# Kernel optimization log

Measured on AMD Instinct MI355X. Metric: run time of the kernel, lower is better.

The kernel has to match this reference:

```python
import jax, jax.numpy as jnp
import numpy as np

THRESH = 0.33
EPS = 1e-10


def _ternarize(x, max_val):
    # x / (max(|x|)+eps) thresholded to {-1, 0, +1}
    n = x / (max_val + EPS)
    return jnp.where(n > THRESH, 1, jnp.where(n < -THRESH, -1, 0)).astype(jnp.int32)


def setup_inputs() -> dict:
    key = jax.random.key(0)
    k1, k2 = jax.random.split(key)
    V, D = 131072, 1024
    qs = jax.random.normal(k1, (D,), dtype=jnp.float32)
    # embedding init: xavier-ish normal + small noise, then row-normalized (as in _initialize_embeddings)
    W = jax.random.normal(k2, (V, D), dtype=jnp.float32)
    W = W / jnp.linalg.norm(W, axis=1, keepdims=True)
    return {"quantum_state": qs, "embedding_weight": W, "top_k": 16}


def reference(quantum_state, embedding_weight, top_k):
    V, D = embedding_weight.shape
    # --- coarse pass: ternary quantization of query and full table ---
    t_state = _ternarize(quantum_state, jnp.max(jnp.abs(quantum_state)))          # [D]
    t_emb = _ternarize(embedding_weight,
                       jnp.max(jnp.abs(embedding_weight), axis=1, keepdims=True))  # [V,D]
    eq = (t_state[None, :] == t_emb)                                               # [V,D]
    # matches contribute +1, mismatches -0.5 (matches.sum - 0.5*mismatches.sum)
    ternary_sim = jnp.sum(jnp.where(eq, 1.0, -0.5), axis=1)                        # [V]
    k3 = min(top_k * 3, V)
    _, top_ternary_idx = jax.lax.top_k(ternary_sim, k3)                            # [k3]
    # --- refine pass: cosine similarity on candidates ---
    cand = embedding_weight[top_ternary_idx]                                       # [k3,D]
    q_n = quantum_state / (jnp.linalg.norm(quantum_state) + 1e-12)
    c_n = cand / (jnp.linalg.norm(cand, axis=1, keepdims=True) + 1e-12)
    refined = c_n @ q_n                                                            # [k3]
    top_scores, top_local = jax.lax.top_k(refined, top_k)                          # [top_k]
    top_global = top_ternary_idx[top_local]
    return top_scores, top_global
```

## Files before the change

### kernel.cpp

```cpp
#include <hip/hip_runtime.h>
#include <stdint.h>

#define VROWS 131072
#define DIM   1024
#define TTHRESH 0.33f
#define TEPS    1e-10f
#define KB_BLOCKS 2048
#define REG_BLOCKS 832
#define NHB   32
#define CAP   16384
#define CAPL  4096

#define MBOUND ((double)TTHRESH + 0x1p-26)

#define GCOUNT_OFF 1024
#define TVAL_OFF  1028
#define MATCH_OFF 4096
#define PART_OFF  (MATCH_OFF + 4 * VROWS)
#define KEYS_OFF  ((PART_OFF + 4 * NHB * 1025 + 7) & ~7)

typedef float f32x4 __attribute__((ext_vector_type(4)));

__device__ __forceinline__ float max4abs(f32x4 a) {
    return fmaxf(fmaxf(fabsf(a.x), fabsf(a.y)), fmaxf(fabsf(a.z), fabsf(a.w)));
}

__device__ __forceinline__ float boundary(float d) {
    double md = MBOUND * (double)d;
    float r = (float)md;
    if (!((double)r >= md)) r = __int_as_float(__float_as_int(r) + 1);
    return r;
}

#define SLOT(x, j) { \
    unsigned long long bp = __ballot((x) >= r); \
    unsigned long long bn = __ballot((x) <= nr); \
    unsigned long long b0 = ~(bp | bn); \
    cnt += (int)__popcll((bp & MP[j]) | (bn & MN[j]) | (b0 & ~(MP[j] | MN[j]))); }

template <bool NT>
__device__ __forceinline__ f32x4 ldW(const f32x4* p) {
    if (NT) return __builtin_nontemporal_load(p);
    return *p;
}

template <bool NT>
__device__ __forceinline__ void rows16(const float* __restrict__ W, int row0, int lane,
                                       const unsigned long long* MP, const unsigned long long* MN,
                                       int* __restrict__ matches) {
    const f32x4* p = (const f32x4*)(W + (size_t)row0 * DIM) + lane;
    f32x4 c0 = ldW<NT>(p), c1 = ldW<NT>(p + 64), c2 = ldW<NT>(p + 128), c3 = ldW<NT>(p + 192);
    f32x4 n0 = c0, n1 = c1, n2 = c2, n3 = c3;
#pragma unroll 1
    for (int i = 0; i < 16; ++i) {
        if (i < 15) {
            const f32x4* pn = (const f32x4*)(W + (size_t)(row0 + i + 1) * DIM) + lane;
            n0 = ldW<NT>(pn); n1 = ldW<NT>(pn + 64); n2 = ldW<NT>(pn + 128); n3 = ldW<NT>(pn + 192);
        }
        float m = fmaxf(fmaxf(max4abs(c0), max4abs(c1)), fmaxf(max4abs(c2), max4abs(c3)));
        for (int s = 1; s < 64; s <<= 1) m = fmaxf(m, __shfl_xor(m, s));
        float r = boundary(m + TEPS), nr = -r;
        int cnt = 0;
        SLOT(c0.x, 0)  SLOT(c0.y, 1)  SLOT(c0.z, 2)  SLOT(c0.w, 3)
        SLOT(c1.x, 4)  SLOT(c1.y, 5)  SLOT(c1.z, 6)  SLOT(c1.w, 7)
        SLOT(c2.x, 8)  SLOT(c2.y, 9)  SLOT(c2.z, 10) SLOT(c2.w, 11)
        SLOT(c3.x, 12) SLOT(c3.y, 13) SLOT(c3.z, 14) SLOT(c3.w, 15)
        if (lane == 0) matches[row0 + i] = cnt;
        c0 = n0; c1 = n1; c2 = n2; c3 = n3;
    }
}

__global__ __launch_bounds__(256, 8) void kB_coarse(const float* __restrict__ W,
                                                    const float* __restrict__ q,
                                                    int* __restrict__ matches) {
    int t = threadIdx.x;
    int wave = t >> 6, lane = t & 63;

    const f32x4* q4 = (const f32x4*)q;
    f32x4 qv0 = q4[lane], qv1 = q4[64 + lane], qv2 = q4[128 + lane], qv3 = q4[192 + lane];
    float mq = fmaxf(fmaxf(max4abs(qv0), max4abs(qv1)), fmaxf(max4abs(qv2), max4abs(qv3)));
    for (int s = 1; s < 64; s <<= 1) mq = fmaxf(mq, __shfl_xor(mq, s));
    float rq = boundary(mq + TEPS), nrq = -rq;
    unsigned long long MP[16], MN[16];
#pragma unroll
    for (int j = 0; j < 4; ++j) {
        f32x4 v = (j == 0) ? qv0 : (j == 1) ? qv1 : (j == 2) ? qv2 : qv3;
        MP[j * 4 + 0] = __ballot(v.x >= rq);  MN[j * 4 + 0] = __ballot(v.x <= nrq);
        MP[j * 4 + 1] = __ballot(v.y >= rq);  MN[j * 4 + 1] = __ballot(v.y <= nrq);
        MP[j * 4 + 2] = __ballot(v.z >= rq);  MN[j * 4 + 2] = __ballot(v.z <= nrq);
        MP[j * 4 + 3] = __ballot(v.w >= rq);  MN[j * 4 + 3] = __ballot(v.w <= nrq);
    }

    int bb = (blockIdx.x * 997) & (KB_BLOCKS - 1);
    int row0 = bb * 64 + wave * 16;
    if (bb < REG_BLOCKS) {
        rows16<false>(W, row0, lane, MP, MN, matches);
    } else {
        rows16<true>(W, row0, lane, MP, MN, matches);
    }
}

__global__ __launch_bounds__(1024) void kHist(const int* __restrict__ matches,
                                              int* __restrict__ partials,
                                              int* __restrict__ gcount) {
    __shared__ int h[1025];
    int t = threadIdx.x;
    if (t == 0) h[1024] = 0;
    if (blockIdx.x == 0 && t == 0) *gcount = 0;
    h[t] = 0;
    __syncthreads();
    int gid = blockIdx.x * 1024 + t;
    int4 m4 = ((const int4*)matches)[gid];
    atomicAdd(&h[m4.x], 1);
    atomicAdd(&h[m4.y], 1);
    atomicAdd(&h[m4.z], 1);
    atomicAdd(&h[m4.w], 1);
    __syncthreads();
    int* dst = partials + blockIdx.x * 1025;
    dst[t] = h[t];
    if (t == 0) dst[1024] = h[1024];
}

__global__ __launch_bounds__(1024) void kGather(const int* __restrict__ matches,
                                                const int* __restrict__ partials,
                                                const int* __restrict__ topk,
                                                unsigned long long* __restrict__ keys,
                                                int* __restrict__ gcount,
                                                int* __restrict__ tval) {
    __shared__ int S[2048];
    __shared__ int sT;
    int t = threadIdx.x;

    int K = *topk;
    if (K < 1) K = 1;
    if (K > 64) K = 64;
    int k3 = 3 * K;
    if (k3 > VROWS) k3 = VROWS;

    int hb = 0, hb1 = 0;
    for (int k = 0; k < NHB; ++k) {
        hb += partials[k * 1025 + t];
        if (t == 0) hb1 += partials[k * 1025 + 1024];
    }
    S[t] = hb;
    S[1024 + t] = (t == 0) ? hb1 : 0;
    __syncthreads();

    for (int s = 1; s < 2048; s <<= 1) {
        int a = S[t] + ((t + s < 2048) ? S[t + s] : 0);
        int b = S[1024 + t] + ((1024 + t + s < 2048) ? S[1024 + t + s] : 0);
        __syncthreads();
        S[t] = a;
        S[1024 + t] = b;
        __syncthreads();
    }
    if (S[t] >= k3 && S[t + 1] < k3) sT = t;
    if (t == 0 && S[1024] >= k3) sT = 1024;
    __syncthreads();
    int T = sT;
    if (t == 0) *tval = T;

    int j = blockIdx.x * 1024 + t;
    int4 m4 = ((const int4*)matches)[j];
    int rbase = j * 4;
    if (m4.x >= T) { int p = atomicAdd(gcount, 1); if (p < CAP) keys[p] = ((unsigned long long)m4.x << 32) | (unsigned int)(~(rbase)); }
    if (m4.y >= T) { int p = atomicAdd(gcount, 1); if (p < CAP) keys[p] = ((unsigned long long)m4.y << 32) | (unsigned int)(~(rbase + 1)); }
    if (m4.z >= T) { int p = atomicAdd(gcount, 1); if (p < CAP) keys[p] = ((unsigned long long)m4.z << 32) | (unsigned int)(~(rbase + 2)); }
    if (m4.w >= T) { int p = atomicAdd(gcount, 1); if (p < CAP) keys[p] = ((unsigned long long)m4.w << 32) | (unsigned int)(~(rbase + 3)); }
}

__global__ __launch_bounds__(1024) void kF_final(const float* __restrict__ W,
                                                 const float* __restrict__ q,
                                                 const int* __restrict__ topk,
                                                 const int* __restrict__ matches,
                                                 const unsigned long long* __restrict__ keys,
                                                 const int* __restrict__ gcount,
                                                 const int* __restrict__ tval,
                                                 float* __restrict__ out) {
    __shared__ __align__(16) float qs[DIM];
    __shared__ float redf[1024];
    __shared__ unsigned long long kl[CAPL];
    __shared__ int sel[192];
    __shared__ float refined[192];
    __shared__ float sQn;
    __shared__ int sG;
    int t = threadIdx.x;

    if (t < 256) ((float4*)qs)[t] = ((const float4*)q)[t];
    __syncthreads();

    float qv = qs[t];
    redf[t] = qv * qv;
    __syncthreads();
    for (int s = 512; s > 0; s >>= 1) {
        if (t < s) redf[t] += redf[t + s];
        __syncthreads();
    }
    if (t == 0) sQn = sqrtf(redf[0]) + 1e-12f;

    int K = *topk;
    if (K < 1) K = 1;
    if (K > 64) K = 64;
    int k3 = 3 * K;
    if (k3 > VROWS) k3 = VROWS;

    int G = *gcount;
    if (G <= CAPL) {
        if (t < G) kl[t] = keys[t];
        if (t == 0) sG = G;
    } else {
        if (t == 0) {
            int T = *tval;
            int n = 0;
            for (int v = 0; v < VROWS && n < k3; ++v)
                if (matches[v] > T) kl[n++] = ((unsigned long long)matches[v] << 32) | (unsigned int)(~v);
            for (int v = 0; v < VROWS && n < k3; ++v)
                if (matches[v] == T) kl[n++] = ((unsigned long long)matches[v] << 32) | (unsigned int)(~v);
            sG = n;
        }
    }
    __syncthreads();
    G = sG;

    for (int i = t; i < G; i += 1024) {
        unsigned long long ki = kl[i];
        int rank = 0;
        for (int j = 0; j < G; ++j) rank += (kl[j] > ki) ? 1 : 0;
        if (rank < k3) sel[rank] = (int)(~(unsigned int)ki);
    }
    __syncthreads();

    int wave = t >> 6, lane = t & 63;
    float qn = sQn;
    for (int i = wave; i < k3; i += 16) {
        int row = sel[i];
        const float4* Wr = (const float4*)(W + (size_t)row * DIM);
        float dot = 0.f, ss = 0.f;
        for (int j2 = 0; j2 < 4; ++j2) {
            float4 a = Wr[j2 * 64 + lane];
            float4 b = ((const float4*)qs)[j2 * 64 + lane];
            dot += a.x * b.x + a.y * b.y + a.z * b.z + a.w * b.w;
            ss  += a.x * a.x + a.y * a.y + a.z * a.z + a.w * a.w;
        }
        for (int s = 1; s < 64; s <<= 1) {
            dot += __shfl_xor(dot, s);
            ss  += __shfl_xor(ss, s);
        }
        if (lane == 0) refined[i] = dot / ((sqrtf(ss) + 1e-12f) * qn);
    }
    __syncthreads();

    if (t < k3) {
        float rv = refined[t];
        int rank = 0;
        for (int j = 0; j < k3; ++j)
            rank += ((refined[j] > rv) || (refined[j] == rv && j < t)) ? 1 : 0;
        if (rank < K) {
            out[rank] = rv;
            out[K + rank] = (float)sel[t];
        }
    }
}

extern "C" void kernel_launch(void* const* d_in, const int* in_sizes, int n_in,
                              void* d_out, int out_size, void* d_ws, size_t ws_size,
                              hipStream_t stream) {
    const float* q = (const float*)d_in[0];
    const float* W = (const float*)d_in[1];
    const int* topk = (const int*)d_in[2];
    float* out = (float*)d_out;
    char* ws = (char*)d_ws;

    int* gcount = (int*)(ws + GCOUNT_OFF);
    int* tval = (int*)(ws + TVAL_OFF);
    int* matches = (int*)(ws + MATCH_OFF);
    int* partials = (int*)(ws + PART_OFF);
    unsigned long long* keys = (unsigned long long*)(ws + KEYS_OFF);

    kB_coarse<<<KB_BLOCKS, 256, 0, stream>>>(W, q, matches);
    kHist<<<NHB, 1024, 0, stream>>>(matches, partials, gcount);
    kGather<<<NHB, 1024, 0, stream>>>(matches, partials, topk, keys, gcount, tval);
    kF_final<<<1, 1024, 0, stream>>>(W, q, topk, matches, keys, gcount, tval, out);
}
```

Before: 108.3 us.

## Fuse histogram, gather and final selection into one cooperative kernel

Merges the three post-coarse kernels (histogram, threshold gather, final refine/top-k) into a single cooperative launch with grid-wide syncs, removing two kernel launch boundaries. The matches vector is loaded once and reused across the hist and gather phases. It also raises the split point between register-path and the other rows16 variant in the coarse kernel. Cooperative launch adds grid.sync overhead, and the large shared-memory footprint per block (now combining all three kernels' buffers) may limit co-residency.

Result: slower. 134.9 us (+24.5%).

```diff
diff --git a/kernel.cpp b/kernel.cpp
--- a/kernel.cpp
+++ b/kernel.cpp
@@ -1,12 +1,15 @@
 #include <hip/hip_runtime.h>
+#include <hip/hip_cooperative_groups.h>
 #include <stdint.h>
+
+namespace cg = cooperative_groups;
 
 #define VROWS 131072
 #define DIM   1024
 #define TTHRESH 0.33f
 #define TEPS    1e-10f
 #define KB_BLOCKS 2048
-#define REG_BLOCKS 832
+#define REG_BLOCKS 960
 #define NHB   32
 #define CAP   16384
 #define CAPL  4096
@@ -100,42 +103,52 @@
     }
 }
 
-__global__ __launch_bounds__(1024) void kHist(const int* __restrict__ matches,
-                                              int* __restrict__ partials,
-                                              int* __restrict__ gcount) {
+__global__ __launch_bounds__(1024) void kS_select(const float* __restrict__ W,
+                                                  const float* __restrict__ q,
+                                                  const int* __restrict__ topk,
+                                                  const int* __restrict__ matches,
+                                                  int* __restrict__ partials,
+                                                  unsigned long long* __restrict__ keys,
+                                                  int* __restrict__ gcount,
+                                                  int* __restrict__ tval,
+                                                  float* __restrict__ out) {
+    cg::grid_group grid = cg::this_grid();
     __shared__ int h[1025];
+    __shared__ int S[2048];
+    __shared__ __align__(16) float qs[DIM];
+    __shared__ float redf[1024];
+    __shared__ unsigned long long kl[CAPL];
+    __shared__ int sel[192];
+    __shared__ float refined[192];
+    __shared__ int sT;
+    __shared__ float sQn;
+    __shared__ int sG;
     int t = threadIdx.x;
+    int b = blockIdx.x;
+
+    int K = *topk;
+    if (K < 1) K = 1;
+    if (K > 64) K = 64;
+    int k3 = 3 * K;
+    if (k3 > VROWS) k3 = VROWS;
+
     if (t == 0) h[1024] = 0;
-    if (blockIdx.x == 0 && t == 0) *gcount = 0;
+    if (b == 0 && t == 0) *gcount = 0;
     h[t] = 0;
     __syncthreads();
-    int gid = blockIdx.x * 1024 + t;
+    int gid = b * 1024 + t;
     int4 m4 = ((const int4*)matches)[gid];
     atomicAdd(&h[m4.x], 1);
     atomicAdd(&h[m4.y], 1);
     atomicAdd(&h[m4.z], 1);
     atomicAdd(&h[m4.w], 1);
     __syncthreads();
-    int* dst = partials + blockIdx.x * 1025;
-    dst[t] = h[t];
-    if (t == 0) dst[1024] = h[1024];
-}
-
-__global__ __launch_bounds__(1024) void kGather(const int* __restrict__ matches,
-                                                const int* __restrict__ partials,
-                                                const int* __restrict__ topk,
-                                                unsigned long long* __restrict__ keys,
-                                                int* __restrict__ gcount,
-                                                int* __restrict__ tval) {
-    __shared__ int S[2048];
-    __shared__ int sT;
-    int t = threadIdx.x;
-
-    int K = *topk;
-    if (K < 1) K = 1;
-    if (K > 64) K = 64;
-    int k3 = 3 * K;
-    if (k3 > VROWS) k3 = VROWS;
+    {
+        int* dst = partials + b * 1025;
+        dst[t] = h[t];
+        if (t == 0) dst[1024] = h[1024];
+    }
+    grid.sync();
 
     int hb = 0, hb1 = 0;
     for (int k = 0; k < NHB; ++k) {
@@ -145,50 +158,33 @@
     S[t] = hb;
     S[1024 + t] = (t == 0) ? hb1 : 0;
     __syncthreads();
-
     for (int s = 1; s < 2048; s <<= 1) {
         int a = S[t] + ((t + s < 2048) ? S[t + s] : 0);
-        int b = S[1024 + t] + ((1024 + t + s < 2048) ? S[1024 + t + s] : 0);
+        int bsum = S[1024 + t] + ((1024 + t + s < 2048) ? S[1024 + t + s] : 0);
         __syncthreads();
         S[t] = a;
-        S[1024 + t] = b;
+        S[1024 + t] = bsum;
         __syncthreads();
     }
     if (S[t] >= k3 && S[t + 1] < k3) sT = t;
     if (t == 0 && S[1024] >= k3) sT = 1024;
     __syncthreads();
     int T = sT;
-    if (t == 0) *tval = T;
-
-    int j = blockIdx.x * 1024 + t;
-    int4 m4 = ((const int4*)matches)[j];
-    int rbase = j * 4;
-    if (m4.x >= T) { int p = atomicAdd(gcount, 1); if (p < CAP) keys[p] = ((unsigned long long)m4.x << 32) | (unsigned int)(~(rbase)); }
-    if (m4.y >= T) { int p = atomicAdd(gcount, 1); if (p < CAP) keys[p] = ((unsigned long long)m4.y << 32) | (unsigned int)(~(rbase + 1)); }
-    if (m4.z >= T) { int p = atomicAdd(gcount, 1); if (p < CAP) keys[p] = ((unsigned long long)m4.z << 32) | (unsigned int)(~(rbase + 2)); }
-    if (m4.w >= T) { int p = atomicAdd(gcount, 1); if (p < CAP) keys[p] = ((unsigned long long)m4.w << 32) | (unsigned int)(~(rbase + 3)); }
-}
-
-__global__ __launch_bounds__(1024) void kF_final(const float* __restrict__ W,
-                                                 const float* __restrict__ q,
-                                                 const int* __restrict__ topk,
-                                                 const int* __restrict__ matches,
-                                                 const unsigned long long* __restrict__ keys,
-                                                 const int* __restrict__ gcount,
-                                                 const int* __restrict__ tval,
-                                                 float* __restrict__ out) {
-    __shared__ __align__(16) float qs[DIM];
-    __shared__ float redf[1024];
-    __shared__ unsigned long long kl[CAPL];
-    __shared__ int sel[192];
-    __shared__ float refined[192];
-    __shared__ float sQn;
-    __shared__ int sG;
-    int t = threadIdx.x;
+    if (b == 0 && t == 0) *tval = T;
+
+    {
+        int rbase = gid * 4;
+        if (m4.x >= T) { int p = atomicAdd(gcount, 1); if (p < CAP) keys[p] = ((unsigned long long)m4.x << 32) | (unsigned int)(~(rbase)); }
+        if (m4.y >= T) { int p = atomicAdd(gcount, 1); if (p < CAP) keys[p] = ((unsigned long long)m4.y << 32) | (unsigned int)(~(rbase + 1)); }
+        if (m4.z >= T) { int p = atomicAdd(gcount, 1); if (p < CAP) keys[p] = ((unsigned long long)m4.z << 32) | (unsigned int)(~(rbase + 2)); }
+        if (m4.w >= T) { int p = atomicAdd(gcount, 1); if (p < CAP) keys[p] = ((unsigned long long)m4.w << 32) | (unsigned int)(~(rbase + 3)); }
+    }
+    grid.sync();
+
+    if (b != 0) return;
 
     if (t < 256) ((float4*)qs)[t] = ((const float4*)q)[t];
     __syncthreads();
-
     float qv = qs[t];
     redf[t] = qv * qv;
     __syncthreads();
@@ -197,12 +193,6 @@
         __syncthreads();
     }
     if (t == 0) sQn = sqrtf(redf[0]) + 1e-12f;
-
-    int K = *topk;
-    if (K < 1) K = 1;
-    if (K > 64) K = 64;
-    int k3 = 3 * K;
-    if (k3 > VROWS) k3 = VROWS;
 
     int G = *gcount;
     if (G <= CAPL) {
@@ -210,12 +200,12 @@
         if (t == 0) sG = G;
     } else {
         if (t == 0) {
-            int T = *tval;
+            int TT = *tval;
             int n = 0;
             for (int v = 0; v < VROWS && n < k3; ++v)
-                if (matches[v] > T) kl[n++] = ((unsigned long long)matches[v] << 32) | (unsigned int)(~v);
+                if (matches[v] > TT) kl[n++] = ((unsigned long long)matches[v] << 32) | (unsigned int)(~v);
             for (int v = 0; v < VROWS && n < k3; ++v)
-                if (matches[v] == T) kl[n++] = ((unsigned long long)matches[v] << 32) | (unsigned int)(~v);
+                if (matches[v] == TT) kl[n++] = ((unsigned long long)matches[v] << 32) | (unsigned int)(~v);
             sG = n;
         }
     }
@@ -238,8 +228,8 @@
         float dot = 0.f, ss = 0.f;
         for (int j2 = 0; j2 < 4; ++j2) {
             float4 a = Wr[j2 * 64 + lane];
-            float4 b = ((const float4*)qs)[j2 * 64 + lane];
-            dot += a.x * b.x + a.y * b.y + a.z * b.z + a.w * b.w;
+            float4 bq = ((const float4*)qs)[j2 * 64 + lane];
+            dot += a.x * bq.x + a.y * bq.y + a.z * bq.z + a.w * bq.w;
             ss  += a.x * a.x + a.y * a.y + a.z * a.z + a.w * a.w;
         }
         for (int s = 1; s < 64; s <<= 1) {
@@ -278,7 +268,9 @@
     unsigned long long* keys = (unsigned long long*)(ws + KEYS_OFF);
 
     kB_coarse<<<KB_BLOCKS, 256, 0, stream>>>(W, q, matches);
-    kHist<<<NHB, 1024, 0, stream>>>(matches, partials, gcount);
-    kGather<<<NHB, 1024, 0, stream>>>(matches, partials, topk, keys, gcount, tval);
-    kF_final<<<1, 1024, 0, stream>>>(W, q, topk, matches, keys, gcount, tval, out);
-}
+
+    const int* matches_c = matches;
+    void* kargs[] = {(void*)&W, (void*)&q, (void*)&topk, (void*)&matches_c,
+                     (void*)&partials, (void*)&keys, (void*)&gcount, (void*)&tval, (void*)&out};
+    hipLaunchCooperativeKernel((void*)kS_select, dim3(NHB), dim3(1024), kargs, 0, stream);
+}
```
